# Optimization experiments

Hardware: AMD Instinct MI355X
Metric: run time of the kernel (lower is better)

Reference implementation:

```python
import jax, jax.numpy as jnp
import numpy as np

B, OBS, H, M, L1, T, A = 16384, 376, 512, 8, 3, 50, 17  # L1 = num_layers - 1
LOG_SQRT_2PI = 0.5 * np.log(2.0 * np.pi).astype(np.float32)


def setup_inputs() -> dict:
    key = jax.random.key(0)
    ks = jax.random.split(key, 16)
    s = lambda fan: 1.0 / np.sqrt(fan).astype(np.float32)
    return {
        "x": jax.random.normal(ks[0], (B, OBS), jnp.float32),
        "task_idx": jax.random.randint(ks[1], (B,), 0, T, jnp.int64),
        "enc_W1": jax.random.normal(ks[2], (OBS, H), jnp.float32) * s(OBS),
        "enc_b1": jnp.zeros((H,), jnp.float32),
        "enc_W2": jax.random.normal(ks[3], (H, H), jnp.float32) * s(H),
        "enc_b2": jnp.zeros((H,), jnp.float32),
        "task_emb": jax.random.normal(ks[4], (T, H), jnp.float32),
        "a_rW": jax.random.normal(ks[5], (L1, H, M * M), jnp.float32) * s(H),
        "a_rb": jnp.zeros((L1, M * M), jnp.float32),
        "c_rW": jax.random.normal(ks[6], (L1, H, M * M), jnp.float32) * s(H),
        "c_rb": jnp.zeros((L1, M * M), jnp.float32),
        "a_W": jax.random.normal(ks[7], (L1, M, H, H), jnp.float32) * s(H),
        "a_b": jnp.zeros((L1, M, H), jnp.float32),
        "a_Wf": jax.random.normal(ks[8], (M, H, A), jnp.float32) * 0.01,
        "a_bf": jnp.zeros((M, A), jnp.float32),
        "c_W": jax.random.normal(ks[9], (L1, M, H, H), jnp.float32) * s(H),
        "c_b": jnp.zeros((L1, M, H), jnp.float32),
        "c_Wf": jax.random.normal(ks[10], (M, H, 1), jnp.float32) * s(H),
        "c_bf": jnp.zeros((M, 1), jnp.float32),
        "actor_logstd": jnp.zeros((1, A), jnp.float32),
    }


def _routing(context, rW, rb):
    # context: [B,H]; rW: [L1,H,M*M] -> list of [B,M,M] softmax routing probs
    rel = jax.nn.relu(context)
    probs = []
    for l in range(L1):
        logits = (rel @ rW[l] + rb[l]).reshape(-1, M, M)
        probs.append(jax.nn.softmax(logits, axis=2))
    return probs


def _base(f_s, probs, W, b, Wf, bf):
    # f_s: [B,H]; W: [L1,M,H,H]; Wf: [M,H,out]
    g = jnp.broadcast_to(f_s[:, None, :], (f_s.shape[0], M, H))  # [B,M,H]
    for l in range(L1):
        outs = jax.nn.relu(jnp.einsum("bmh,mhk->bmk", g, W[l]) + b[l])  # [B,M,H]
        g = jnp.einsum("bij,bjh->bih", probs[l], outs)  # soft combine
    final = jnp.einsum("bmh,mhk->bmk", g, Wf) + bf  # [B,M,out]
    return final.sum(axis=1)


def reference(x, task_idx, enc_W1, enc_b1, enc_W2, enc_b2, task_emb,
              a_rW, a_rb, c_rW, c_rb, a_W, a_b, a_Wf, a_bf,
              c_W, c_b, c_Wf, c_bf, actor_logstd):
    f_s = jnp.tanh(jnp.tanh(x @ enc_W1 + enc_b1) @ enc_W2 + enc_b2)  # [B,H]
    h_z = task_emb[task_idx]  # [B,H]
    context = f_s * h_z

    value = _base(f_s, _routing(context, c_rW, c_rb), c_W, c_b, c_Wf, c_bf)  # [B,1]
    mean = _base(f_s, _routing(context, a_rW, a_rb), a_W, a_b, a_Wf, a_bf)   # [B,A]

    # deterministic action (sample=False): action = mean
    logstd = jnp.broadcast_to(actor_logstd, mean.shape)
    log_prob = (-logstd - LOG_SQRT_2PI).sum(axis=1)          # N.log_prob(mean).sum(1)
    entropy = (0.5 + LOG_SQRT_2PI + logstd).sum(axis=1)
    # concat (action, log_prob, entropy, value) -> [B, A+3]
    return jnp.concatenate([mean, log_prob[:, None], entropy[:, None], value], axis=1)
```

## Files before the change

### kernel.cpp

```cpp
#include <hip/hip_runtime.h>
#include <hip/hip_bf16.h>

typedef float f32x4 __attribute__((ext_vector_type(4)));
typedef float f32x2 __attribute__((ext_vector_type(2)));
typedef int   i32x4 __attribute__((ext_vector_type(4)));
typedef int   i32x8 __attribute__((ext_vector_type(8)));

#define LOG_SQRT_2PI 0.91893853320467274f

static constexpr int BSZ  = 16384;
static constexpr int OBSN = 376;
static constexpr int HD   = 512;
static constexpr int NACT = 17;

__device__ __forceinline__ unsigned char f2fp8(float v) {
  return (unsigned char)(__builtin_amdgcn_cvt_pk_fp8_f32(v, v, 0, false) & 0xFF);
}

__device__ __forceinline__ void xcd_map(int id, int gx, int gy, int& bx, int& by, int& bz) {
  int p = id & 7, l = id >> 3;
  bx = l % gx;
  int g = (l / gx) * 8 + p;
  by = g % gy;
  bz = g / gy;
}


__global__ void k_cvt_pad8(const float* __restrict__ src, unsigned char* __restrict__ dst) {
  long i = (long)blockIdx.x * 256 + threadIdx.x;
  if (i >= (long)BSZ * HD) return;
  long r = i >> 9;
  int  c = (int)(i & 511);
  dst[i] = f2fp8(c < OBSN ? src[r * OBSN + c] : 0.f);
}

__global__ void k_packT8(const float* __restrict__ src, unsigned char* __restrict__ dst,
                         int K, int N, int Kpad, long sstride, long dstride, float scale) {
  __shared__ float t[32][33];
  src += (long)blockIdx.z * sstride;
  dst += (long)blockIdx.z * dstride;
  int k0 = blockIdx.y * 32, n0 = blockIdx.x * 32;
#pragma unroll
  for (int ii = 0; ii < 4; ++ii) {
    int i = ii * 8 + threadIdx.y;
    int k = k0 + i, n = n0 + threadIdx.x;
    t[i][threadIdx.x] = (k < K && n < N) ? src[(long)k * N + n] : 0.f;
  }
  __syncthreads();
#pragma unroll
  for (int ii = 0; ii < 4; ++ii) {
    int i = ii * 8 + threadIdx.y;
    int n = n0 + i, k = k0 + threadIdx.x;
    if (n < N && k < Kpad) dst[(long)n * Kpad + k] = f2fp8(scale * t[threadIdx.x][i]);
  }
}

__global__ void k_packw8(const float* __restrict__ aW, const float* __restrict__ cW,
                         unsigned char* __restrict__ dst) {
  __shared__ float t[32][33];
  const int z = blockIdx.z;
  const float* src = (z < 24) ? aW + (long)z * 262144 : cW + (long)(z - 24) * 262144;
  unsigned char* d = dst + (long)z * 262144;
  int k0 = blockIdx.y * 32, n0 = blockIdx.x * 32;
#pragma unroll
  for (int ii = 0; ii < 4; ++ii) {
    int i = ii * 8 + threadIdx.y;
    t[i][threadIdx.x] = src[(long)(k0 + i) * 512 + n0 + threadIdx.x];
  }
  __syncthreads();
#pragma unroll
  for (int ii = 0; ii < 4; ++ii) {
    int i = ii * 8 + threadIdx.y;
    d[(long)(n0 + i) * 512 + k0 + threadIdx.x] = f2fp8(16.f * t[threadIdx.x][i]);
  }
}

__global__ void k_packwf8(const float* __restrict__ aWf, const float* __restrict__ cWf,
                          unsigned char* __restrict__ dsta, unsigned char* __restrict__ dstc) {
  int i = blockIdx.x * 256 + threadIdx.x;
  int n = i >> 12, k = i & 4095;
  dsta[i] = (n < NACT) ? f2fp8(64.f * aWf[(long)k * NACT + n]) : (unsigned char)0;
  dstc[i] = (n < 1)    ? f2fp8(64.f * cWf[k])                  : (unsigned char)0;
}

__global__ void k_pack_rb(const float* __restrict__ a_rb, const float* __restrict__ c_rb,
                          float* __restrict__ rb) {
  int i = threadIdx.x;
  rb[i] = (i < 192) ? a_rb[i] : c_rb[i - 192];
}

__global__ void k_sum_bf(const float* __restrict__ a_bf, const float* __restrict__ c_bf,
                         float* __restrict__ sa, float* __restrict__ sc) {
  int a = threadIdx.x;
  if (a < NACT) { float s = 0.f; for (int m = 0; m < 8; ++m) s += a_bf[m * NACT + a]; sa[a] = s; }
  if (a == 0)   { float s = 0.f; for (int m = 0; m < 8; ++m) s += c_bf[m];            sc[0] = s; }
}

template <int OP>
__global__ __launch_bounds__(256)
void k_gemm8(const unsigned char* __restrict__ A, const unsigned char* __restrict__ Bt,
             void* __restrict__ Cv, const float* __restrict__ bias,
             int N, int K, int lda, int ldc, int gx, int gy,
             int a_zoff, int b_zoff, int c_zoff, int bias_zoff,
             const int* __restrict__ tidx, const float* __restrict__ temb,
             unsigned char* __restrict__ out2) {
  __shared__ alignas(16) unsigned char sA[128 * 128];
  __shared__ alignas(16) unsigned char sB[128 * 128];
  int bx, by, z;
  xcd_map(blockIdx.x, gx, gy, bx, by, z);
  A  += (long)z * a_zoff;
  Bt += (long)z * b_zoff;
  const int tid  = threadIdx.x;
  const int wave = tid >> 6, lane = tid & 63;
  const int wr = (wave >> 1) * 64, wc = (wave & 1) * 64;
  const int row0 = by * 128, col0 = bx * 128;
  const int lcol = lane & 15, quad = lane >> 4;
  const int sw7 = lcol & 7;
  const int c0 = ((2 * quad)     ^ sw7) * 16;
  const int c1 = ((2 * quad + 1) ^ sw7) * 16;

  f32x4 acc[4][4] = {};

  for (int kt = 0; kt < K; kt += 128) {
#pragma unroll
    for (int i = 0; i < 4; ++i) {
      int u = i * 256 + tid;
      int r = u >> 3, gc = (u & 7) ^ (r & 7);
      const unsigned char* ga = A + (long)(row0 + r) * lda + kt + gc * 16;
      __builtin_amdgcn_global_load_lds((const __attribute__((address_space(1))) void*)ga,
                                       (__attribute__((address_space(3))) void*)&sA[u * 16], 16, 0, 0);
    }
#pragma unroll
    for (int i = 0; i < 4; ++i) {
      int u = i * 256 + tid;
      int r = u >> 3, gc = (u & 7) ^ (r & 7);
      const unsigned char* gb = Bt + (long)(col0 + r) * K + kt + gc * 16;
      __builtin_amdgcn_global_load_lds((const __attribute__((address_space(1))) void*)gb,
                                       (__attribute__((address_space(3))) void*)&sB[u * 16], 16, 0, 0);
    }
    __syncthreads();
    i32x8 af[4], bv[4];
#pragma unroll
    for (int t = 0; t < 4; ++t) {
      int ra = (wr + t * 16 + lcol) * 128;
      int rb = (wc + t * 16 + lcol) * 128;
      i32x4 alo = *(const i32x4*)&sA[ra + c0];
      i32x4 ahi = *(const i32x4*)&sA[ra + c1];
      i32x4 blo = *(const i32x4*)&sB[rb + c0];
      i32x4 bhi = *(const i32x4*)&sB[rb + c1];
      af[t] = (i32x8){alo[0], alo[1], alo[2], alo[3], ahi[0], ahi[1], ahi[2], ahi[3]};
      bv[t] = (i32x8){blo[0], blo[1], blo[2], blo[3], bhi[0], bhi[1], bhi[2], bhi[3]};
    }
#pragma unroll
    for (int mi = 0; mi < 4; ++mi)
#pragma unroll
      for (int ni = 0; ni < 4; ++ni)
        acc[mi][ni] = __builtin_amdgcn_mfma_scale_f32_16x16x128_f8f6f4(
            bv[ni], af[mi], acc[mi][ni], 0, 0, 0, 0x7F, 0, 0x7F);
    __syncthreads();
  }

#pragma unroll
  for (int ni = 0; ni < 4; ++ni) {
    int colb = col0 + wc + ni * 16 + quad * 4;
    if (colb >= N) continue;
    float4 bw = *(const float4*)&bias[(long)z * bias_zoff + colb];
#pragma unroll
    for (int mi = 0; mi < 4; ++mi) {
      int rowg = row0 + wr + mi * 16 + lcol;
      float v0 = acc[mi][ni][0] * 0.0625f + bw.x;
      float v1 = acc[mi][ni][1] * 0.0625f + bw.y;
      float v2 = acc[mi][ni][2] * 0.0625f + bw.z;
      float v3 = acc[mi][ni][3] * 0.0625f + bw.w;
      long idx = (long)rowg * ldc + (long)z * c_zoff + colb;
      if (OP == 0) {
        unsigned d = __builtin_amdgcn_cvt_pk_fp8_f32(fmaxf(v0, 0.f), fmaxf(v1, 0.f), 0, false);
        d = __builtin_amdgcn_cvt_pk_fp8_f32(fmaxf(v2, 0.f), fmaxf(v3, 0.f), d, true);
        *(unsigned*)&((unsigned char*)Cv)[idx] = d;
      } else if (OP == 1) {
        float t0 = tanhf(v0), t1 = tanhf(v1), t2 = tanhf(v2), t3 = tanhf(v3);
        unsigned d = __builtin_amdgcn_cvt_pk_fp8_f32(t0, t1, 0, false);
        d = __builtin_amdgcn_cvt_pk_fp8_f32(t2, t3, d, true);
        *(unsigned*)&((unsigned char*)Cv)[idx] = d;
      } else if (OP == 5) {
        float t0 = tanhf(v0), t1 = tanhf(v1), t2 = tanhf(v2), t3 = tanhf(v3);
        unsigned d = __builtin_amdgcn_cvt_pk_fp8_f32(t0, t1, 0, false);
        d = __builtin_amdgcn_cvt_pk_fp8_f32(t2, t3, d, true);
        *(unsigned*)&((unsigned char*)Cv)[idx] = d;
        int tk = tidx[rowg];
        float4 te = *(const float4*)&temb[(long)tk * HD + colb];
        unsigned e = __builtin_amdgcn_cvt_pk_fp8_f32(fmaxf(t0 * te.x, 0.f), fmaxf(t1 * te.y, 0.f), 0, false);
        e = __builtin_amdgcn_cvt_pk_fp8_f32(fmaxf(t2 * te.z, 0.f), fmaxf(t3 * te.w, 0.f), e, true);
        *(unsigned*)&out2[idx] = e;
      } else if (OP == 4) {
        float mx = fmaxf(fmaxf(v0, v1), fmaxf(v2, v3));
        mx = fmaxf(mx, __shfl_xor(mx, 16));
        float e0 = __expf(v0 - mx), e1 = __expf(v1 - mx), e2 = __expf(v2 - mx), e3 = __expf(v3 - mx);
        float s = e0 + e1 + e2 + e3;
        s += __shfl_xor(s, 16);
        float inv = 1.f / s;
        *(float4*)&((float*)Cv)[idx] = make_float4(e0 * inv, e1 * inv, e2 * inv, e3 * inv);
      }
    }
  }
}

__global__ __launch_bounds__(256)
void k_combine8(const unsigned char* __restrict__ outs, const float* __restrict__ probs,
                unsigned char* __restrict__ g, int poff) {
  __shared__ float P[4][64];
  const int w = threadIdx.x >> 6, l = threadIdx.x & 63;
  const long b = (long)blockIdx.x * 4 + w;
  P[w][l] = probs[b * 384 + poff + l];
  __syncthreads();
  const unsigned char* ob = outs + b * 4096 + l * 8;
  float o[8][8];
#pragma unroll
  for (int j = 0; j < 8; ++j) {
    uint2 v = *(const uint2*)(ob + j * 512);
    f32x2 p01 = __builtin_amdgcn_cvt_pk_f32_fp8(v.x, false);
    f32x2 p23 = __builtin_amdgcn_cvt_pk_f32_fp8(v.x, true);
    f32x2 p45 = __builtin_amdgcn_cvt_pk_f32_fp8(v.y, false);
    f32x2 p67 = __builtin_amdgcn_cvt_pk_f32_fp8(v.y, true);
    o[j][0] = p01.x; o[j][1] = p01.y; o[j][2] = p23.x; o[j][3] = p23.y;
    o[j][4] = p45.x; o[j][5] = p45.y; o[j][6] = p67.x; o[j][7] = p67.y;
  }
  unsigned char* gb = g + b * 4096 + l * 8;
#pragma unroll
  for (int i = 0; i < 8; ++i) {
    float a[8] = {};
#pragma unroll
    for (int j = 0; j < 8; ++j) {
      float pw = P[w][i * 8 + j];
#pragma unroll
      for (int c = 0; c < 8; ++c) a[c] += pw * o[j][c];
    }
    unsigned int lo = __builtin_amdgcn_cvt_pk_fp8_f32(a[0], a[1], 0, false);
    lo = __builtin_amdgcn_cvt_pk_fp8_f32(a[2], a[3], lo, true);
    unsigned int hi = __builtin_amdgcn_cvt_pk_fp8_f32(a[4], a[5], 0, false);
    hi = __builtin_amdgcn_cvt_pk_fp8_f32(a[6], a[7], hi, true);
    *(uint2*)(gb + i * 512) = make_uint2(lo, hi);
  }
}

template <int NOUT>
__global__ __launch_bounds__(256)
void k_head8(const unsigned char* __restrict__ A, const unsigned char* __restrict__ Bt,
             const float* __restrict__ bsum, float* __restrict__ out, int ooff) {
  __shared__ alignas(16) unsigned char sA[64 * 64];
  __shared__ alignas(16) unsigned char sB[32 * 64];
  const int tid = threadIdx.x;
  const int wave = tid >> 6, lane = tid & 63;
  const int row0 = blockIdx.x * 64;
  const int lcol = lane & 15, quad = lane >> 4;
  const int sw = (lcol >> 1) & 3;
  const int co0 = (((quad >> 1)    ) ^ sw) * 16 + (quad & 1) * 8;
  const int co1 = (((quad >> 1) + 2) ^ sw) * 16 + (quad & 1) * 8;
  f32x4 acc[2] = {};

  for (int kt = 0; kt < 4096; kt += 64) {
    {
      int r = tid >> 2, gc = (tid & 3) ^ ((tid >> 3) & 3);
      const unsigned char* ga = A + (long)(row0 + r) * 4096 + kt + gc * 16;
      __builtin_amdgcn_global_load_lds((const __attribute__((address_space(1))) void*)ga,
                                       (__attribute__((address_space(3))) void*)&sA[tid * 16], 16, 0, 0);
    }
    if (tid < 128) {
      int r = tid >> 2, gc = (tid & 3) ^ ((tid >> 3) & 3);
      const unsigned char* gb = Bt + (long)r * 4096 + kt + gc * 16;
      __builtin_amdgcn_global_load_lds((const __attribute__((address_space(1))) void*)gb,
                                       (__attribute__((address_space(3))) void*)&sB[tid * 16], 16, 0, 0);
    }
    __syncthreads();
    long af[2], bv[2][2];
    int ra = (wave * 16 + lcol) * 64;
    af[0] = *(const long*)&sA[ra + co0];
    af[1] = *(const long*)&sA[ra + co1];
#pragma unroll
    for (int ni = 0; ni < 2; ++ni) {
      int rb = (ni * 16 + lcol) * 64;
      bv[0][ni] = *(const long*)&sB[rb + co0];
      bv[1][ni] = *(const long*)&sB[rb + co1];
    }
#pragma unroll
    for (int kk = 0; kk < 2; ++kk)
#pragma unroll
      for (int ni = 0; ni < 2; ++ni)
        acc[ni] = __builtin_amdgcn_mfma_f32_16x16x32_fp8_fp8(af[kk], bv[kk][ni], acc[ni], 0, 0, 0);
    __syncthreads();
  }

#pragma unroll
  for (int ni = 0; ni < 2; ++ni) {
    int col = ni * 16 + lcol;
    if (col >= NOUT) continue;
#pragma unroll
    for (int r = 0; r < 4; ++r) {
      int row = row0 + wave * 16 + quad * 4 + r;
      out[(long)row * 20 + ooff + col] = acc[ni][r] * 0.015625f + bsum[col];
    }
  }
}

__global__ void k_logstd(const float* __restrict__ ls, float* __restrict__ out) {
  float lp = 0.f, ent = 0.f;
#pragma unroll
  for (int a = 0; a < NACT; ++a) {
    float v = ls[a];
    lp  += -v - LOG_SQRT_2PI;
    ent += 0.5f + LOG_SQRT_2PI + v;
  }
  long b = (long)blockIdx.x * 256 + threadIdx.x;
  if (b < BSZ) { out[b * 20 + 17] = lp; out[b * 20 + 18] = ent; }
}


extern "C" void kernel_launch(void* const* d_in, const int* in_sizes, int n_in,
                              void* d_out, int out_size, void* d_ws, size_t ws_size,
                              hipStream_t stream) {
  const float* x        = (const float*)d_in[0];
  const int*   task_idx = (const int*)d_in[1];
  const float* enc_W1   = (const float*)d_in[2];
  const float* enc_b1   = (const float*)d_in[3];
  const float* enc_W2   = (const float*)d_in[4];
  const float* enc_b2   = (const float*)d_in[5];
  const float* task_emb = (const float*)d_in[6];
  const float* a_rW     = (const float*)d_in[7];
  const float* a_rb     = (const float*)d_in[8];
  const float* c_rW     = (const float*)d_in[9];
  const float* c_rb     = (const float*)d_in[10];
  const float* a_W      = (const float*)d_in[11];
  const float* a_b      = (const float*)d_in[12];
  const float* a_Wf     = (const float*)d_in[13];
  const float* a_bf     = (const float*)d_in[14];
  const float* c_W      = (const float*)d_in[15];
  const float* c_b      = (const float*)d_in[16];
  const float* c_Wf     = (const float*)d_in[17];
  const float* c_bf     = (const float*)d_in[18];
  const float* logstd   = (const float*)d_in[19];
  float* out = (float*)d_out;

  char* ws = (char*)d_ws;
  size_t off = 0;
  auto carve = [&](size_t bytes) {
    char* p = ws + off;
    off += (bytes + 255) & ~(size_t)255;
    return p;
  };
  unsigned char* W8 = (unsigned char*)carve((size_t)48 * 262144);
  unsigned char* W1T8 = (unsigned char*)carve((size_t)512 * 512);
  unsigned char* W2T8 = (unsigned char*)carve((size_t)512 * 512);
  unsigned char* rWT8 = (unsigned char*)carve((size_t)384 * 512);
  float* rball = (float*)carve(384 * 4);
  unsigned char* WfaT8 = (unsigned char*)carve((size_t)32 * 4096);
  unsigned char* WfcT8 = (unsigned char*)carve((size_t)32 * 4096);
  float* bfa   = (float*)carve(128 * 4);
  float* bfc   = (float*)carve(128 * 4);
  unsigned char* fs8 = (unsigned char*)carve((size_t)BSZ * HD);
  float* lgt   = (float*)carve((size_t)BSZ * 384 * 4);

  size_t remain = (ws_size > off) ? (ws_size - off) : 0;
  int Bc = 4096;
  for (int cand = BSZ; cand > 4096; cand >>= 1)
    if ((size_t)2 * cand * 4096 <= remain) { Bc = cand; break; }
  size_t half = (size_t)Bc * 4096;
  unsigned char* bufA8 = (unsigned char*)carve(half);
  unsigned char* bufB8 = (unsigned char*)carve(half);
  unsigned char* x8   = bufA8;
  unsigned char* h18  = bufB8;
  unsigned char* rel8 = bufA8;

  dim3 tb(32, 8);

  k_cvt_pad8<<<(int)(((long)BSZ * HD + 255) / 256), 256, 0, stream>>>(x, x8);
  k_packT8<<<dim3(16, 16, 1), tb, 0, stream>>>(enc_W1, W1T8, OBSN, 512, 512, 0, 0, 16.f);
  k_packT8<<<dim3(16, 16, 1), tb, 0, stream>>>(enc_W2, W2T8, 512, 512, 512, 0, 0, 16.f);
  k_packT8<<<dim3(2, 16, 3),  tb, 0, stream>>>(a_rW, rWT8,             512, 64, 512, 512 * 64, 64 * 512, 16.f);
  k_packT8<<<dim3(2, 16, 3),  tb, 0, stream>>>(c_rW, rWT8 + 192 * 512, 512, 64, 512, 512 * 64, 64 * 512, 16.f);
  k_packw8<<<dim3(16, 16, 48), tb, 0, stream>>>(a_W, c_W, W8);
  k_packwf8<<<512, 256, 0, stream>>>(a_Wf, c_Wf, WfaT8, WfcT8);
  k_pack_rb<<<1, 384, 0, stream>>>(a_rb, c_rb, rball);
  k_sum_bf<<<1, 32, 0, stream>>>(a_bf, c_bf, bfa, bfc);

  const int GY = BSZ / 128;
  k_gemm8<1><<<4 * GY, 256, 0, stream>>>(x8, W1T8, h18, enc_b1, 512, 512, 512, 512,
                                         4, GY, 0, 0, 0, 0, nullptr, nullptr, nullptr);
  k_gemm8<5><<<4 * GY, 256, 0, stream>>>(h18, W2T8, fs8, enc_b2, 512, 512, 512, 512,
                                         4, GY, 0, 0, 0, 0, task_idx, task_emb, rel8);
  k_gemm8<4><<<3 * GY, 256, 0, stream>>>(rel8, rWT8, lgt, rball, 384, 512, 512, 384,
                                         3, GY, 0, 0, 0, 0, nullptr, nullptr, nullptr);

  const size_t wz8 = (size_t)8 * 262144;
  const unsigned char* W8a = W8;
  const unsigned char* W8c = W8 + (size_t)24 * 262144;
  for (int c0 = 0; c0 < BSZ; c0 += Bc) {
    const unsigned char* fs_c = fs8 + (long)c0 * 512;
    const float* pr_c  = lgt + (long)c0 * 384;
    float*       out_c = out + (long)c0 * 20;
    const int gy = Bc / 128;

    k_gemm8<0><<<32 * gy, 256, 0, stream>>>(fs_c, W8c, bufA8, c_b, 4096, 512, 512, 4096,
                                            32, gy, 0, 0, 0, 0, nullptr, nullptr, nullptr);
    k_combine8<<<Bc / 4, 256, 0, stream>>>(bufA8, pr_c, bufB8, 192 + 0);
    k_gemm8<0><<<4 * gy * 8, 256, 0, stream>>>(bufB8, W8c + 1 * wz8, bufA8, c_b + 4096,
                                               512, 512, 4096, 4096, 4, gy, 512, 262144, 512, 512,
                                               nullptr, nullptr, nullptr);
    k_combine8<<<Bc / 4, 256, 0, stream>>>(bufA8, pr_c, bufB8, 192 + 64);
    k_gemm8<0><<<4 * gy * 8, 256, 0, stream>>>(bufB8, W8c + 2 * wz8, bufA8, c_b + 8192,
                                               512, 512, 4096, 4096, 4, gy, 512, 262144, 512, 512,
                                               nullptr, nullptr, nullptr);
    k_combine8<<<Bc / 4, 256, 0, stream>>>(bufA8, pr_c, bufB8, 192 + 128);
    k_head8<1><<<Bc / 64, 256, 0, stream>>>(bufB8, WfcT8, bfc, out_c, 19);

    k_gemm8<0><<<32 * gy, 256, 0, stream>>>(fs_c, W8a, bufA8, a_b, 4096, 512, 512, 4096,
                                            32, gy, 0, 0, 0, 0, nullptr, nullptr, nullptr);
    k_combine8<<<Bc / 4, 256, 0, stream>>>(bufA8, pr_c, bufB8, 0);
    k_gemm8<0><<<4 * gy * 8, 256, 0, stream>>>(bufB8, W8a + 1 * wz8, bufA8, a_b + 4096,
                                               512, 512, 4096, 4096, 4, gy, 512, 262144, 512, 512,
                                               nullptr, nullptr, nullptr);
    k_combine8<<<Bc / 4, 256, 0, stream>>>(bufA8, pr_c, bufB8, 64);
    k_gemm8<0><<<4 * gy * 8, 256, 0, stream>>>(bufB8, W8a + 2 * wz8, bufA8, a_b + 8192,
                                               512, 512, 4096, 4096, 4, gy, 512, 262144, 512, 512,
                                               nullptr, nullptr, nullptr);
    k_combine8<<<Bc / 4, 256, 0, stream>>>(bufA8, pr_c, bufB8, 128);
    k_head8<NACT><<<Bc / 64, 256, 0, stream>>>(bufB8, WfaT8, bfa, out_c, 0);
  }

  k_logstd<<<BSZ / 256, 256, 0, stream>>>(logstd, out);
}
```

Baseline: 806.7 us.

## Add 256x256-tile FP8 GEMM with async LDS loads for expert layers

Adds a new k_gemm256 kernel that computes 256x256 output tiles with 512 threads (8 waves, each 128x64). It double-buffers 128-wide K slices into swizzled LDS via global_load_lds and raises wave priority around the MFMA bursts. All six per-chunk expert GEMMs now use it in place of the 128-tile k_gemm8<0>, and the OP==0 epilogue branch is dropped from k_gemm8. The larger tile increases operand reuse per LDS byte and cuts global traffic. In exchange it uses 128 KB of LDS per block and launches fewer blocks, which can hurt occupancy and load balance.

```diff
diff --git a/kernel.cpp b/kernel.cpp
--- a/kernel.cpp
+++ b/kernel.cpp
@@ -173,11 +173,7 @@
       float v2 = acc[mi][ni][2] * 0.0625f + bw.z;
       float v3 = acc[mi][ni][3] * 0.0625f + bw.w;
       long idx = (long)rowg * ldc + (long)z * c_zoff + colb;
-      if (OP == 0) {
-        unsigned d = __builtin_amdgcn_cvt_pk_fp8_f32(fmaxf(v0, 0.f), fmaxf(v1, 0.f), 0, false);
-        d = __builtin_amdgcn_cvt_pk_fp8_f32(fmaxf(v2, 0.f), fmaxf(v3, 0.f), d, true);
-        *(unsigned*)&((unsigned char*)Cv)[idx] = d;
-      } else if (OP == 1) {
+      if (OP == 1) {
         float t0 = tanhf(v0), t1 = tanhf(v1), t2 = tanhf(v2), t3 = tanhf(v3);
         unsigned d = __builtin_amdgcn_cvt_pk_fp8_f32(t0, t1, 0, false);
         d = __builtin_amdgcn_cvt_pk_fp8_f32(t2, t3, d, true);
@@ -201,6 +197,96 @@
         float inv = 1.f / s;
         *(float4*)&((float*)Cv)[idx] = make_float4(e0 * inv, e1 * inv, e2 * inv, e3 * inv);
       }
+    }
+  }
+}
+
+__global__ __launch_bounds__(512, 2)
+void k_gemm256(const unsigned char* __restrict__ A, const unsigned char* __restrict__ Bt,
+               unsigned char* __restrict__ C, const float* __restrict__ bias,
+               int K, int lda, int ldc, int gx, int gy,
+               int a_zoff, int b_zoff, int c_zoff, int bias_zoff) {
+  __shared__ alignas(16) unsigned char sA[2][256 * 128];
+  __shared__ alignas(16) unsigned char sB[2][256 * 128];
+  int bx, by, z;
+  xcd_map(blockIdx.x, gx, gy, bx, by, z);
+  A  += (long)z * a_zoff;
+  Bt += (long)z * b_zoff;
+  const int tid  = threadIdx.x;
+  const int wave = tid >> 6, lane = tid & 63;
+  const int wr = (wave >> 2) * 128;
+  const int wc = (wave & 3) * 64;
+  const int row0 = by * 256, col0 = bx * 256;
+  const int lcol = lane & 15, quad = lane >> 4;
+  const int sw7 = lcol & 7;
+  const int c0 = ((2 * quad)     ^ sw7) * 16;
+  const int c1 = ((2 * quad + 1) ^ sw7) * 16;
+
+  f32x4 acc[8][4] = {};
+
+  auto stage = [&](int kt, int p) {
+#pragma unroll
+    for (int i = 0; i < 4; ++i) {
+      int u = i * 512 + tid;
+      int r = u >> 3, gc = (u & 7) ^ (r & 7);
+      const unsigned char* ga = A + (long)(row0 + r) * lda + kt + gc * 16;
+      __builtin_amdgcn_global_load_lds((const __attribute__((address_space(1))) void*)ga,
+                                       (__attribute__((address_space(3))) void*)&sA[p][u * 16], 16, 0, 0);
+    }
+#pragma unroll
+    for (int i = 0; i < 4; ++i) {
+      int u = i * 512 + tid;
+      int r = u >> 3, gc = (u & 7) ^ (r & 7);
+      const unsigned char* gb = Bt + (long)(col0 + r) * K + kt + gc * 16;
+      __builtin_amdgcn_global_load_lds((const __attribute__((address_space(1))) void*)gb,
+                                       (__attribute__((address_space(3))) void*)&sB[p][u * 16], 16, 0, 0);
+    }
+  };
+
+  stage(0, 0);
+  __syncthreads();
+  int p = 0;
+  for (int kt = 0; kt < K; kt += 128) {
+    if (kt + 128 < K) stage(kt + 128, p ^ 1);
+    i32x8 bv[4];
+#pragma unroll
+    for (int ni = 0; ni < 4; ++ni) {
+      int rb = (wc + ni * 16 + lcol) * 128;
+      i32x4 blo = *(const i32x4*)&sB[p][rb + c0];
+      i32x4 bhi = *(const i32x4*)&sB[p][rb + c1];
+      bv[ni] = (i32x8){blo[0], blo[1], blo[2], blo[3], bhi[0], bhi[1], bhi[2], bhi[3]};
+    }
+#pragma unroll
+    for (int mi = 0; mi < 8; ++mi) {
+      int ra = (wr + mi * 16 + lcol) * 128;
+      i32x4 alo = *(const i32x4*)&sA[p][ra + c0];
+      i32x4 ahi = *(const i32x4*)&sA[p][ra + c1];
+      i32x8 af = (i32x8){alo[0], alo[1], alo[2], alo[3], ahi[0], ahi[1], ahi[2], ahi[3]};
+      __builtin_amdgcn_s_setprio(1);
+#pragma unroll
+      for (int ni = 0; ni < 4; ++ni)
+        acc[mi][ni] = __builtin_amdgcn_mfma_scale_f32_16x16x128_f8f6f4(
+            bv[ni], af, acc[mi][ni], 0, 0, 0, 0x7F, 0, 0x7F);
+      __builtin_amdgcn_s_setprio(0);
+    }
+    __syncthreads();
+    p ^= 1;
+  }
+
+#pragma unroll
+  for (int ni = 0; ni < 4; ++ni) {
+    int colb = col0 + wc + ni * 16 + quad * 4;
+    float4 bw = *(const float4*)&bias[(long)z * bias_zoff + colb];
+#pragma unroll
+    for (int mi = 0; mi < 8; ++mi) {
+      int rowg = row0 + wr + mi * 16 + lcol;
+      float v0 = fmaxf(acc[mi][ni][0] * 0.0625f + bw.x, 0.f);
+      float v1 = fmaxf(acc[mi][ni][1] * 0.0625f + bw.y, 0.f);
+      float v2 = fmaxf(acc[mi][ni][2] * 0.0625f + bw.z, 0.f);
+      float v3 = fmaxf(acc[mi][ni][3] * 0.0625f + bw.w, 0.f);
+      unsigned d = __builtin_amdgcn_cvt_pk_fp8_f32(v0, v1, 0, false);
+      d = __builtin_amdgcn_cvt_pk_fp8_f32(v2, v3, d, true);
+      *(unsigned*)&C[(long)rowg * ldc + (long)z * c_zoff + colb] = d;
     }
   }
 }
@@ -397,31 +483,27 @@
     const unsigned char* fs_c = fs8 + (long)c0 * 512;
     const float* pr_c  = lgt + (long)c0 * 384;
     float*       out_c = out + (long)c0 * 20;
-    const int gy = Bc / 128;
-
-    k_gemm8<0><<<32 * gy, 256, 0, stream>>>(fs_c, W8c, bufA8, c_b, 4096, 512, 512, 4096,
-                                            32, gy, 0, 0, 0, 0, nullptr, nullptr, nullptr);
+    const int gy = Bc / 256;
+
+    k_gemm256<<<16 * gy, 512, 0, stream>>>(fs_c, W8c, bufA8, c_b, 512, 512, 4096,
+                                           16, gy, 0, 0, 0, 0);
     k_combine8<<<Bc / 4, 256, 0, stream>>>(bufA8, pr_c, bufB8, 192 + 0);
-    k_gemm8<0><<<4 * gy * 8, 256, 0, stream>>>(bufB8, W8c + 1 * wz8, bufA8, c_b + 4096,
-                                               512, 512, 4096, 4096, 4, gy, 512, 262144, 512, 512,
-                                               nullptr, nullptr, nullptr);
+    k_gemm256<<<2 * gy * 8, 512, 0, stream>>>(bufB8, W8c + 1 * wz8, bufA8, c_b + 4096,
+                                              512, 4096, 4096, 2, gy, 512, 262144, 512, 512);
     k_combine8<<<Bc / 4, 256, 0, stream>>>(bufA8, pr_c, bufB8, 192 + 64);
-    k_gemm8<0><<<4 * gy * 8, 256, 0, stream>>>(bufB8, W8c + 2 * wz8, bufA8, c_b + 8192,
-                                               512, 512, 4096, 4096, 4, gy, 512, 262144, 512, 512,
-                                               nullptr, nullptr, nullptr);
+    k_gemm256<<<2 * gy * 8, 512, 0, stream>>>(bufB8, W8c + 2 * wz8, bufA8, c_b + 8192,
+                                              512, 4096, 4096, 2, gy, 512, 262144, 512, 512);
     k_combine8<<<Bc / 4, 256, 0, stream>>>(bufA8, pr_c, bufB8, 192 + 128);
     k_head8<1><<<Bc / 64, 256, 0, stream>>>(bufB8, WfcT8, bfc, out_c, 19);
 
-    k_gemm8<0><<<32 * gy, 256, 0, stream>>>(fs_c, W8a, bufA8, a_b, 4096, 512, 512, 4096,
-                                            32, gy, 0, 0, 0, 0, nullptr, nullptr, nullptr);
+    k_gemm256<<<16 * gy, 512, 0, stream>>>(fs_c, W8a, bufA8, a_b, 512, 512, 4096,
+                                           16, gy, 0, 0, 0, 0);
     k_combine8<<<Bc / 4, 256, 0, stream>>>(bufA8, pr_c, bufB8, 0);
-    k_gemm8<0><<<4 * gy * 8, 256, 0, stream>>>(bufB8, W8a + 1 * wz8, bufA8, a_b + 4096,
-                                               512, 512, 4096, 4096, 4, gy, 512, 262144, 512, 512,
-                                               nullptr, nullptr, nullptr);
+    k_gemm256<<<2 * gy * 8, 512, 0, stream>>>(bufB8, W8a + 1 * wz8, bufA8, a_b + 4096,
+                                              512, 4096, 4096, 2, gy, 512, 262144, 512, 512);
     k_combine8<<<Bc / 4, 256, 0, stream>>>(bufA8, pr_c, bufB8, 64);
-    k_gemm8<0><<<4 * gy * 8, 256, 0, stream>>>(bufB8, W8a + 2 * wz8, bufA8, a_b + 8192,
-                                               512, 512, 4096, 4096, 4, gy, 512, 262144, 512, 512,
-                                               nullptr, nullptr, nullptr);
+    k_gemm256<<<2 * gy * 8, 512, 0, stream>>>(bufB8, W8a + 2 * wz8, bufA8, a_b + 8192,
+                                              512, 4096, 4096, 2, gy, 512, 262144, 512, 512);
     k_combine8<<<Bc / 4, 256, 0, stream>>>(bufA8, pr_c, bufB8, 128);
     k_head8<NACT><<<Bc / 64, 256, 0, stream>>>(bufB8, WfaT8, bfa, out_c, 0);
   }
```

After: 842.4 us. +4.4%, slower.
